# Kernel optimization log

Measured on AMD Instinct MI355X. Metric: run time of the kernel, lower is better.

Reference implementation:

```python
import jax, jax.numpy as jnp
import numpy as np

B = 128          # batch_size
D = 512          # in_features / hidden_size
V = 10000        # word_length (vocab)
T = 20           # sequence_length


def setup_inputs() -> dict:
    key = jax.random.key(0)
    ks = jax.random.split(key, 11)
    s = 0.02
    return {
        "input_": jax.random.normal(ks[0], (1, B, D), dtype=jnp.float32),
        # layer 0 LSTM: input_size=V, hidden_size=D (torch gate order i,f,g,o)
        "W_ih0": jax.random.normal(ks[1], (4 * D, V), dtype=jnp.float32) * s,
        "W_hh0": jax.random.normal(ks[2], (4 * D, D), dtype=jnp.float32) * s,
        "b_ih0": jax.random.normal(ks[3], (4 * D,), dtype=jnp.float32) * s,
        "b_hh0": jax.random.normal(ks[4], (4 * D,), dtype=jnp.float32) * s,
        # layer 1 LSTM: input_size=D, hidden_size=D
        "W_ih1": jax.random.normal(ks[5], (4 * D, D), dtype=jnp.float32) * s,
        "W_hh1": jax.random.normal(ks[6], (4 * D, D), dtype=jnp.float32) * s,
        "b_ih1": jax.random.normal(ks[7], (4 * D,), dtype=jnp.float32) * s,
        "b_hh1": jax.random.normal(ks[8], (4 * D,), dtype=jnp.float32) * s,
        # state_encoder: Linear(D -> V)
        "W_enc": jax.random.normal(ks[9], (V, D), dtype=jnp.float32) * s,
        "b_enc": jax.random.normal(ks[10], (V,), dtype=jnp.float32) * s,
    }


def _lstm_cell(x, h, c, W_ih, W_hh, b_ih, b_hh):
    # x: (B, In), h/c: (B, H). Torch nn.LSTM gate order: i, f, g, o.
    gates = x @ W_ih.T + h @ W_hh.T + (b_ih + b_hh)
    i, f, g, o = jnp.split(gates, 4, axis=-1)
    c_new = jax.nn.sigmoid(f) * c + jax.nn.sigmoid(i) * jnp.tanh(g)
    h_new = jax.nn.sigmoid(o) * jnp.tanh(c_new)
    return h_new, c_new


def reference(input_, W_ih0, W_hh0, b_ih0, b_hh0,
              W_ih1, W_hh1, b_ih1, b_hh1, W_enc, b_enc):
    # Initial states: H[0] = image features, everything else zero;
    # the first timestep input to layer 0 is zeros(B, V).
    h0 = input_[0]                           # (B, D)
    c0 = jnp.zeros_like(h0)
    h1 = jnp.zeros_like(h0)
    c1 = jnp.zeros_like(h0)
    prev_out = jnp.zeros((h0.shape[0], W_ih0.shape[1]), dtype=h0.dtype)  # (B, V)

    def step(carry, _):
        h0, c0, h1, c1, prev = carry
        h0, c0 = _lstm_cell(prev, h0, c0, W_ih0, W_hh0, b_ih0, b_hh0)
        h1, c1 = _lstm_cell(h0, h1, c1, W_ih1, W_hh1, b_ih1, b_hh1)
        out = h1 @ W_enc.T + b_enc           # state_encoder(H[-1]) -> (B, V)
        return (h0, c0, h1, c1, out), out

    _, outs = jax.lax.scan(step, (h0, c0, h1, c1, prev_out), None, length=T)
    return outs                              # (T, B, V) == torch.cat(dim=0)
```

## Files before the change

### kernel.cpp

```cpp
#include <hip/hip_runtime.h>

typedef __attribute__((ext_vector_type(8))) short short8;
typedef __attribute__((ext_vector_type(4))) short short4v;
typedef __attribute__((ext_vector_type(4))) float floatx4;

#define B_   128
#define D_   512
#define V_   10000
#define T_   20
#define G4   2048
#define VPAD 10112
#define KP2  10240
#define BD   (B_*D_)

__device__ __forceinline__ unsigned short f2b(float x){
  union { float f; unsigned u; } c; c.f = x;
  unsigned u = c.u;
  unsigned r = (u + 0x7fffu + ((u>>16)&1u)) >> 16;
  return (unsigned short)r;
}
__device__ __forceinline__ float sigm(float x){ return 1.0f/(1.0f+__expf(-x)); }

__global__ void k_convert(const float* __restrict__ src, unsigned short* __restrict__ dst, int n){
  int i = blockIdx.x*256 + threadIdx.x;
  if (i < n) dst[i] = f2b(src[i]);
}

__global__ void k_prep(const float* __restrict__ Whh0, const float* __restrict__ Wih1,
                       const float* __restrict__ Whh1, const float* __restrict__ input_,
                       const float* __restrict__ b_ih1, const float* __restrict__ b_hh1,
                       unsigned short* __restrict__ Whh0_b, unsigned short* __restrict__ Wih1_b,
                       unsigned short* __restrict__ Whh1_b, unsigned short* __restrict__ h0b0,
                       float* __restrict__ bias1, float* __restrict__ Mf32,
                       unsigned* __restrict__ bar){
  int i = blockIdx.x*256 + threadIdx.x;
  const int NW = G4*512;
  if (i < NW){
    Whh0_b[i] = f2b(Whh0[i]);
    Wih1_b[i] = f2b(Wih1[i]);
    Whh1_b[i] = f2b(Whh1[i]);
    Mf32[i] = 0.f;
  }
  if (i < BD) h0b0[i] = f2b(input_[i]);
  if (i < 2048) bias1[i] = b_ih1[i] + b_hh1[i];
  if (i < 40*8*16) bar[i] = 0u;
}

__global__ __launch_bounds__(256) void k_trans(const float* __restrict__ Wenc,
    unsigned short* __restrict__ Wenc_b, unsigned short* __restrict__ WencT){
  __shared__ short T[64*72];
  int tid = threadIdx.x;
  int v0 = blockIdx.x * 64;
  int d0 = blockIdx.y * 64;
  #pragma unroll
  for (int i=0;i<4;i++){
    int s = tid + 256*i;
    int row = s >> 4, fq = s & 15;
    int v = v0 + row, d = d0 + fq*4;
    float4 f = {0.f,0.f,0.f,0.f};
    if (v < V_) f = *(const float4*)(Wenc + (long)v*D_ + d);
    short4v h; h[0]=(short)f2b(f.x); h[1]=(short)f2b(f.y); h[2]=(short)f2b(f.z); h[3]=(short)f2b(f.w);
    *(short4v*)(&T[row*72 + fq*4]) = h;
    if (v < VPAD) *(short4v*)(Wenc_b + (long)v*D_ + d) = h;
  }
  __syncthreads();
  #pragma unroll
  for (int i=0;i<2;i++){
    int s = tid + 256*i;
    int drow = s >> 3, oct = s & 7;
    short8 v8;
    #pragma unroll
    for (int j=0;j<8;j++) v8[j] = T[(oct*8+j)*72 + drow];
    *(short8*)(WencT + (long)(d0+drow)*KP2 + v0 + oct*8) = v8;
  }
}

__global__ void k_bias_fold(const float* __restrict__ Wih0, const float* __restrict__ b_enc,
                            const float* __restrict__ b_ih0, const float* __restrict__ b_hh0,
                            float* __restrict__ biasA0, float* __restrict__ bfold){
  __shared__ float red[256];
  int g = blockIdx.x;
  const float* row = Wih0 + (long)g*V_;
  float s = 0.f;
  for (int v = threadIdx.x; v < V_; v += 256) s += row[v]*b_enc[v];
  red[threadIdx.x] = s; __syncthreads();
  for (int w = 128; w >= 1; w >>= 1){
    if (threadIdx.x < w) red[threadIdx.x] += red[threadIdx.x+w];
    __syncthreads();
  }
  if (threadIdx.x == 0){
    float ba = b_ih0[g] + b_hh0[g];
    biasA0[g] = ba;
    bfold[g]  = ba + red[0];
  }
}

__global__ __launch_bounds__(256) void k_fold_gemm(const float* __restrict__ A,
                 const unsigned short* __restrict__ BT, float* __restrict__ Mf32){
  __shared__ short At[128*40];
  __shared__ short Bt[128*40];
  int tid = threadIdx.x;
  int b = blockIdx.x;
  int ks = b >> 6, mn = b & 63;
  int bm = mn >> 2, bn = mn & 3;
  int m0 = bm*128, n0 = bn*128, kb = ks*2560;
  int lane = tid&63, wave = tid>>6, l15 = lane&15, quad = lane>>4;
  int wm = (wave>>1)*64, wn = (wave&1)*64;
  floatx4 acc[4][4];
  #pragma unroll
  for (int i=0;i<4;i++)
    #pragma unroll
    for(int j=0;j<4;j++){ floatx4 z = {0.f,0.f,0.f,0.f}; acc[i][j] = z; }
  for (int it = 0; it < 80; it++){
    int k0 = kb + it*32;
    #pragma unroll
    for (int i=0;i<2;i++){
      int slot = tid + 256*i;
      int row = slot >> 2, oct = slot & 3;
      const float* src = A + (long)(m0+row)*V_ + k0 + oct*8;
      short8 v;
      if (k0 + 32 <= V_){
        float4 f0 = *(const float4*)src;
        float4 f1 = *(const float4*)(src+4);
        v[0]=(short)f2b(f0.x); v[1]=(short)f2b(f0.y); v[2]=(short)f2b(f0.z); v[3]=(short)f2b(f0.w);
        v[4]=(short)f2b(f1.x); v[5]=(short)f2b(f1.y); v[6]=(short)f2b(f1.z); v[7]=(short)f2b(f1.w);
      } else {
        #pragma unroll
        for (int j=0;j<8;j++){
          int kk = k0 + oct*8 + j;
          float x = (kk < V_) ? src[j] : 0.f;
          v[j] = (short)f2b(x);
        }
      }
      *(short8*)(&At[row*40 + oct*8]) = v;
    }
    #pragma unroll
    for (int i=0;i<2;i++){
      int slot = tid + 256*i;
      int row = slot >> 2, oct = slot & 3;
      *(short8*)(&Bt[row*40 + oct*8]) = *(const short8*)(BT + (long)(n0+row)*KP2 + k0 + oct*8);
    }
    __syncthreads();
    short8 af[4], bf[4];
    #pragma unroll
    for (int i=0;i<4;i++){
      af[i] = *(const short8*)(&At[(wm + i*16 + l15)*40 + quad*8]);
      bf[i] = *(const short8*)(&Bt[(wn + i*16 + l15)*40 + quad*8]);
    }
    #pragma unroll
    for (int mi=0;mi<4;mi++)
      #pragma unroll
      for (int ni=0;ni<4;ni++)
        acc[mi][ni] = __builtin_amdgcn_mfma_f32_16x16x32_bf16(af[mi],bf[ni],acc[mi][ni],0,0,0);
    __syncthreads();
  }
  #pragma unroll
  for (int mi=0;mi<4;mi++)
    #pragma unroll
    for (int ni=0;ni<4;ni++){
      int n = n0 + wn + ni*16 + l15;
      #pragma unroll
      for (int r=0;r<4;r++){
        int m = m0 + wm + mi*16 + quad*4 + r;
        atomicAdd(&Mf32[(long)m*D_ + n], acc[mi][ni][r]);
      }
    }
}


#define LSTRIDE 520
#define LDS_TILE (32*LSTRIDE)

__device__ __forceinline__ void wait_phase(const unsigned* __restrict__ bar, int p, int tid){
  if (tid < 64){
    const unsigned* cp = bar + (p*8 + (tid&7))*16;
    bool ok;
    do {
      unsigned v = 16u;
      if (tid < 8) v = __hip_atomic_load(cp, __ATOMIC_RELAXED, __HIP_MEMORY_SCOPE_AGENT);
      ok = __all(v >= 16u) != 0;
      if (!ok) __builtin_amdgcn_s_sleep(1);
    } while (!ok);
  }
  __syncthreads();
  asm volatile("" ::: "memory");
}

__device__ __forceinline__ void arrive_phase(unsigned* __restrict__ bar, int p, int slot, int tid){
  asm volatile("s_waitcnt vmcnt(0) lgkmcnt(0)" ::: "memory");
  __syncthreads();
  if (tid == 0)
    __hip_atomic_fetch_add(bar + (p*8 + slot)*16, 1u, __ATOMIC_RELAXED, __HIP_MEMORY_SCOPE_AGENT);
}

__device__ __forceinline__ void stage_tile(const unsigned short* __restrict__ src,
                                           short* __restrict__ dst, int br0, int tid){
  unsigned long long u[16];
  #pragma unroll
  for (int i=0;i<8;i++){
    int c = tid + 256*i;
    int r = c >> 6, o = c & 63;
    const unsigned long long* p = (const unsigned long long*)(src + (long)(br0 + r)*512 + o*8);
    u[2*i]   = __hip_atomic_load(p,   __ATOMIC_RELAXED, __HIP_MEMORY_SCOPE_SYSTEM);
    u[2*i+1] = __hip_atomic_load(p+1, __ATOMIC_RELAXED, __HIP_MEMORY_SCOPE_SYSTEM);
  }
  #pragma unroll
  for (int i=0;i<8;i++){
    int c = tid + 256*i;
    int r = c >> 6, o = c & 63;
    unsigned long long* q = (unsigned long long*)(dst + r*LSTRIDE + o*8);
    q[0] = u[2*i]; q[1] = u[2*i+1];
  }
}

__global__ __launch_bounds__(256, 1) void k_lstm_all(
    const unsigned short* __restrict__ Mfold, const unsigned short* __restrict__ Whh0,
    const unsigned short* __restrict__ Wih1, const unsigned short* __restrict__ Whh1,
    const float* __restrict__ biasA0, const float* __restrict__ bfold,
    const float* __restrict__ bias1,
    unsigned short* __restrict__ h0b0, unsigned short* __restrict__ h0b1,
    unsigned short* __restrict__ Hs, unsigned* __restrict__ bar)
{
  __shared__ short smem[2*LDS_TILE];
  short* ldsA = smem;
  short* ldsB = smem + LDS_TILE;

  int tid = threadIdx.x;
  int L   = blockIdx.x >> 7;
  int idx = blockIdx.x & 127;
  int jg = idx & 31, bs = idx >> 5;
  int br0 = bs*32, j0 = jg*16;
  int slot = idx & 7;
  int lane = tid & 63, wave = tid >> 6;
  int l15 = lane & 15, quad = lane >> 4;

  const unsigned short* WA = (L==0) ? Mfold : Wih1;
  const unsigned short* WB = (L==0) ? Whh0  : Whh1;
  int gRow = wave*512 + j0 + l15;
  short8 bfa[16], bfb[16];
  #pragma unroll
  for (int ks=0; ks<16; ks++){
    bfa[ks] = *(const short8*)(WA + (long)gRow*512 + ks*32 + quad*8);
    bfb[ks] = *(const short8*)(WB + (long)gRow*512 + ks*32 + quad*8);
  }

  int bl = tid >> 3, jjp = (tid & 7)*2;
  int jglob = j0 + jjp;
  float b0g[4][2], bNg[4][2];
  #pragma unroll
  for (int gg=0; gg<4; gg++)
    #pragma unroll
    for (int q=0; q<2; q++){
      if (L==0){
        b0g[gg][q] = biasA0[gg*512 + jglob + q];
        bNg[gg][q] = bfold [gg*512 + jglob + q];
      } else {
        b0g[gg][q] = bias1 [gg*512 + jglob + q];
        bNg[gg][q] = b0g[gg][q];
      }
    }

  float creg[2] = {0.f, 0.f};
  unsigned short* bufs[2] = {h0b0, h0b1};

  for (int t = 0; t < T_; t++){
    const unsigned short *haP, *hbP; unsigned short* hoP;
    bool hasA, hasB; int p_own, p_oth, p_arr;
    if (L == 0){
      haP = (t>0) ? (Hs + (size_t)(t-1)*BD) : nullptr;
      hbP = bufs[t&1];
      hoP = bufs[(t+1)&1];
      hasA = (t>0); hasB = true;
      p_own = 2*(t-1); p_oth = 2*(t-1)+1; p_arr = 2*t;
    } else {
      haP = bufs[(t+1)&1];
      hbP = (t>0) ? (Hs + (size_t)(t-1)*BD) : nullptr;
      hoP = Hs + (size_t)t*BD;
      hasA = true; hasB = (t>0);
      p_own = 2*(t-1)+1; p_oth = 2*t; p_arr = 2*t+1;
    }

    if (hasB){
      if (t > 0) wait_phase(bar, p_own, tid);
      stage_tile(hbP, ldsB, br0, tid);
    }
    if (hasA){
      wait_phase(bar, p_oth, tid);
      stage_tile(haP, ldsA, br0, tid);
    }
    __syncthreads();

    floatx4 acc[2];
    #pragma unroll
    for (int i=0;i<2;i++){ floatx4 z = {0.f,0.f,0.f,0.f}; acc[i] = z; }
    if (hasA){
      #pragma unroll
      for (int ks=0; ks<16; ks++)
        #pragma unroll
        for (int mt=0; mt<2; mt++){
          short8 a = *(const short8*)(ldsA + (mt*16 + l15)*LSTRIDE + ks*32 + quad*8);
          acc[mt] = __builtin_amdgcn_mfma_f32_16x16x32_bf16(a, bfa[ks], acc[mt], 0,0,0);
        }
    }
    if (hasB){
      #pragma unroll
      for (int ks=0; ks<16; ks++)
        #pragma unroll
        for (int mt=0; mt<2; mt++){
          short8 a = *(const short8*)(ldsB + (mt*16 + l15)*LSTRIDE + ks*32 + quad*8);
          acc[mt] = __builtin_amdgcn_mfma_f32_16x16x32_bf16(a, bfb[ks], acc[mt], 0,0,0);
        }
    }
    __syncthreads();

    float* ex = (float*)smem;
    #pragma unroll
    for (int mt=0; mt<2; mt++)
      #pragma unroll
      for (int r=0; r<4; r++)
        ex[wave*512 + (mt*16 + quad*4 + r)*16 + l15] = acc[mt][r];
    __syncthreads();

    {
      float h2[2];
      #pragma unroll
      for (int q=0; q<2; q++){
        float bi = (t==0) ? b0g[0][q] : bNg[0][q];
        float bf_ = (t==0) ? b0g[1][q] : bNg[1][q];
        float bg = (t==0) ? b0g[2][q] : bNg[2][q];
        float bo = (t==0) ? b0g[3][q] : bNg[3][q];
        float gi = ex[0*512 + bl*16 + jjp+q] + bi;
        float gf = ex[1*512 + bl*16 + jjp+q] + bf_;
        float gg = ex[2*512 + bl*16 + jjp+q] + bg;
        float go = ex[3*512 + bl*16 + jjp+q] + bo;
        float ig = sigm(gi), fg = sigm(gf), gt = tanhf(gg), og = sigm(go);
        float cn = fg*creg[q] + ig*gt;
        creg[q] = cn;
        h2[q] = og*tanhf(cn);
      }
      unsigned pack = (unsigned)f2b(h2[0]) | ((unsigned)f2b(h2[1]) << 16);
      __hip_atomic_store((unsigned*)(hoP + (long)(br0 + bl)*512 + jglob), pack,
                         __ATOMIC_RELAXED, __HIP_MEMORY_SCOPE_SYSTEM);
    }
    arrive_phase(bar, p_arr, slot, tid);
  }
}

__global__ __launch_bounds__(256) void k_out_gemm(
    const unsigned short* __restrict__ Ah,
    const unsigned short* __restrict__ Bw,
    const float* __restrict__ b_enc, float* __restrict__ out)
{
  __shared__ short At[128*40];
  __shared__ short Bt[128*40];
  int tid = threadIdx.x;
  int bm = blockIdx.x % 20, bn = blockIdx.x / 20;
  int m0 = bm*128, n0 = bn*128;
  int lane = tid&63, wave = tid>>6, l15 = lane&15, quad = lane>>4;
  int wm = (wave>>1)*64, wn = (wave&1)*64;
  floatx4 acc[4][4];
  #pragma unroll
  for (int i=0;i<4;i++)
    #pragma unroll
    for(int j=0;j<4;j++){ floatx4 z = {0.f,0.f,0.f,0.f}; acc[i][j] = z; }
  for (int k0=0;k0<512;k0+=32){
    #pragma unroll
    for (int i=0;i<2;i++){
      int cc = tid + 256*i; int row = cc>>2; int ko=(cc&3)*8;
      *(short8*)(&At[row*40+ko]) = *(const short8*)(Ah + (long)(m0+row)*512 + k0+ko);
      *(short8*)(&Bt[row*40+ko]) = *(const short8*)(Bw + (long)(n0+row)*512 + k0+ko);
    }
    __syncthreads();
    short8 af[4], bf[4];
    #pragma unroll
    for (int i=0;i<4;i++){
      af[i] = *(const short8*)(&At[(wm + i*16 + l15)*40 + quad*8]);
      bf[i] = *(const short8*)(&Bt[(wn + i*16 + l15)*40 + quad*8]);
    }
    #pragma unroll
    for (int mi=0;mi<4;mi++)
      #pragma unroll
      for (int ni=0;ni<4;ni++)
        acc[mi][ni] = __builtin_amdgcn_mfma_f32_16x16x32_bf16(af[mi],bf[ni],acc[mi][ni],0,0,0);
    __syncthreads();
  }
  #pragma unroll
  for (int mi=0;mi<4;mi++)
    #pragma unroll
    for (int ni=0;ni<4;ni++){
      int n = n0 + wn + ni*16 + l15;
      if (n < V_){
        float be = b_enc[n];
        #pragma unroll
        for (int r=0;r<4;r++){
          int m = m0 + wm + mi*16 + quad*4 + r;
          out[(long)m*V_ + n] = acc[mi][ni][r] + be;
        }
      }
    }
}

extern "C" void kernel_launch(void* const* d_in, const int* in_sizes, int n_in,
                              void* d_out, int out_size, void* d_ws, size_t ws_size,
                              hipStream_t stream){
  const float* input_ = (const float*)d_in[0];
  const float* W_ih0  = (const float*)d_in[1];
  const float* W_hh0  = (const float*)d_in[2];
  const float* b_ih0  = (const float*)d_in[3];
  const float* b_hh0  = (const float*)d_in[4];
  const float* W_ih1  = (const float*)d_in[5];
  const float* W_hh1  = (const float*)d_in[6];
  const float* b_ih1  = (const float*)d_in[7];
  const float* b_hh1  = (const float*)d_in[8];
  const float* W_enc  = (const float*)d_in[9];
  const float* b_enc  = (const float*)d_in[10];
  float* out = (float*)d_out;

  char* ws = (char*)d_ws;
  size_t off = 0;
  auto alloc = [&](size_t bytes){ void* p = ws + off; off += (bytes + 255) & ~255ull; return p; };
  unsigned short* Wenc_b  = (unsigned short*)alloc((size_t)VPAD*512*2);
  unsigned short* WencT_b = (unsigned short*)alloc((size_t)512*KP2*2);
  float*          Mf32    = (float*)alloc((size_t)G4*512*4);
  unsigned short* Mfold_b = (unsigned short*)alloc((size_t)G4*512*2);
  unsigned short* Whh0_b  = (unsigned short*)alloc((size_t)G4*512*2);
  unsigned short* Wih1_b  = (unsigned short*)alloc((size_t)G4*512*2);
  unsigned short* Whh1_b  = (unsigned short*)alloc((size_t)G4*512*2);
  unsigned short* Hs_b    = (unsigned short*)alloc((size_t)T_*BD*2);
  unsigned short* h0b0    = (unsigned short*)alloc((size_t)BD*2);
  unsigned short* h0b1    = (unsigned short*)alloc((size_t)BD*2);
  float* biasA0 = (float*)alloc(2048*4);
  float* bfold  = (float*)alloc(2048*4);
  float* bias1  = (float*)alloc(2048*4);
  unsigned* bar = (unsigned*)alloc((size_t)40*8*16*4);

  k_prep<<<4096, 256, 0, stream>>>(W_hh0, W_ih1, W_hh1, input_, b_ih1, b_hh1,
                                   Whh0_b, Wih1_b, Whh1_b, h0b0, bias1, Mf32, bar);
  k_trans<<<dim3(KP2/64, 512/64), 256, 0, stream>>>(W_enc, Wenc_b, WencT_b);
  k_bias_fold<<<2048, 256, 0, stream>>>(W_ih0, b_enc, b_ih0, b_hh0, biasA0, bfold);
  k_fold_gemm<<<256, 256, 0, stream>>>(W_ih0, WencT_b, Mf32);
  k_convert<<<(G4*512+255)/256, 256, 0, stream>>>(Mf32, Mfold_b, G4*512);

  {
    const unsigned short* a0 = Mfold_b; const unsigned short* a1 = Whh0_b;
    const unsigned short* a2 = Wih1_b; const unsigned short* a3 = Whh1_b;
    const float* a4 = biasA0; const float* a5 = bfold; const float* a6 = bias1;
    unsigned short* a7 = h0b0; unsigned short* a8 = h0b1; unsigned short* a9 = Hs_b;
    unsigned* a10 = bar;
    void* args[] = {&a0,&a1,&a2,&a3,&a4,&a5,&a6,&a7,&a8,&a9,&a10};
    hipLaunchCooperativeKernel((void*)k_lstm_all, dim3(256), dim3(256), args, 0u, stream);
  }

  k_out_gemm<<<20*79, 256, 0, stream>>>(Hs_b, Wenc_b, b_enc, out);
}
```

Before: 666.2 us.

## Replace counter barriers with per-batch-slice flag waits and overlap recurrent MFMA

The LSTM phase barrier is rewritten so each block sets its own flag per phase and batch slice, and waiters check only the 32 flags of their 32-row batch slice instead of global counters summed over all blocks. The recurrent (own-layer) matmul now starts as soon as its input is ready, before waiting on the other layer's input, so more compute overlaps the wait. The fold GEMM block index mapping is also reordered for better L2 locality. This narrows dependencies and may cut stall time, but uses system-scope flag loads and more flag memory.

```diff
diff --git a/kernel.cpp b/kernel.cpp
--- a/kernel.cpp
+++ b/kernel.cpp
@@ -43,7 +43,7 @@
   }
   if (i < BD) h0b0[i] = f2b(input_[i]);
   if (i < 2048) bias1[i] = b_ih1[i] + b_hh1[i];
-  if (i < 40*8*16) bar[i] = 0u;
+  if (i < 40*4*32) bar[i] = 0u;
 }
 
 __global__ __launch_bounds__(256) void k_trans(const float* __restrict__ Wenc,
@@ -101,8 +101,10 @@
   __shared__ short Bt[128*40];
   int tid = threadIdx.x;
   int b = blockIdx.x;
-  int ks = b >> 6, mn = b & 63;
-  int bm = mn >> 2, bn = mn & 3;
+  int x = b & 7;
+  int bn = (b >> 3) & 3;
+  int idx = (b >> 5) * 8 + x;
+  int bm = idx & 15, ks = idx >> 4;
   int m0 = bm*128, n0 = bn*128, kb = ks*2560;
   int lane = tid&63, wave = tid>>6, l15 = lane&15, quad = lane>>4;
   int wm = (wave>>1)*64, wn = (wave&1)*64;
@@ -128,8 +130,8 @@
         #pragma unroll
         for (int j=0;j<8;j++){
           int kk = k0 + oct*8 + j;
-          float x = (kk < V_) ? src[j] : 0.f;
-          v[j] = (short)f2b(x);
+          float xx = (kk < V_) ? src[j] : 0.f;
+          v[j] = (short)f2b(xx);
         }
       }
       *(short8*)(&At[row*40 + oct*8]) = v;
@@ -171,14 +173,13 @@
 #define LSTRIDE 520
 #define LDS_TILE (32*LSTRIDE)
 
-__device__ __forceinline__ void wait_phase(const unsigned* __restrict__ bar, int p, int tid){
+__device__ __forceinline__ void wait_flags(const unsigned* __restrict__ fl, int tid){
   if (tid < 64){
-    const unsigned* cp = bar + (p*8 + (tid&7))*16;
     bool ok;
     do {
-      unsigned v = 16u;
-      if (tid < 8) v = __hip_atomic_load(cp, __ATOMIC_RELAXED, __HIP_MEMORY_SCOPE_AGENT);
-      ok = __all(v >= 16u) != 0;
+      unsigned v = 1u;
+      if (tid < 32) v = __hip_atomic_load(fl + tid, __ATOMIC_RELAXED, __HIP_MEMORY_SCOPE_SYSTEM);
+      ok = (__all(v != 0u) != 0);
       if (!ok) __builtin_amdgcn_s_sleep(1);
     } while (!ok);
   }
@@ -186,11 +187,11 @@
   asm volatile("" ::: "memory");
 }
 
-__device__ __forceinline__ void arrive_phase(unsigned* __restrict__ bar, int p, int slot, int tid){
+__device__ __forceinline__ void set_flag(unsigned* __restrict__ fp, int tid){
   asm volatile("s_waitcnt vmcnt(0) lgkmcnt(0)" ::: "memory");
   __syncthreads();
   if (tid == 0)
-    __hip_atomic_fetch_add(bar + (p*8 + slot)*16, 1u, __ATOMIC_RELAXED, __HIP_MEMORY_SCOPE_AGENT);
+    __hip_atomic_store(fp, 1u, __ATOMIC_RELAXED, __HIP_MEMORY_SCOPE_SYSTEM);
 }
 
 __device__ __forceinline__ void stage_tile(const unsigned short* __restrict__ src,
@@ -230,7 +231,6 @@
   int idx = blockIdx.x & 127;
   int jg = idx & 31, bs = idx >> 5;
   int br0 = bs*32, j0 = jg*16;
-  int slot = idx & 7;
   int lane = tid & 63, wave = tid >> 6;
   int l15 = lane & 15, quad = lane >> 4;
 
@@ -280,35 +280,32 @@
       p_own = 2*(t-1)+1; p_oth = 2*t; p_arr = 2*t+1;
     }
 
+    floatx4 acc[2];
+    #pragma unroll
+    for (int i=0;i<2;i++){ floatx4 z = {0.f,0.f,0.f,0.f}; acc[i] = z; }
+
     if (hasB){
-      if (t > 0) wait_phase(bar, p_own, tid);
+      if (t > 0) wait_flags(bar + (p_own*4 + bs)*32, tid);
       stage_tile(hbP, ldsB, br0, tid);
+      __syncthreads();
+      #pragma unroll
+      for (int ks=0; ks<16; ks++)
+        #pragma unroll
+        for (int mt=0; mt<2; mt++){
+          short8 a = *(const short8*)(ldsB + (mt*16 + l15)*LSTRIDE + ks*32 + quad*8);
+          acc[mt] = __builtin_amdgcn_mfma_f32_16x16x32_bf16(a, bfb[ks], acc[mt], 0,0,0);
+        }
     }
     if (hasA){
-      wait_phase(bar, p_oth, tid);
+      wait_flags(bar + (p_oth*4 + bs)*32, tid);
       stage_tile(haP, ldsA, br0, tid);
-    }
-    __syncthreads();
-
-    floatx4 acc[2];
-    #pragma unroll
-    for (int i=0;i<2;i++){ floatx4 z = {0.f,0.f,0.f,0.f}; acc[i] = z; }
-    if (hasA){
+      __syncthreads();
       #pragma unroll
       for (int ks=0; ks<16; ks++)
         #pragma unroll
         for (int mt=0; mt<2; mt++){
           short8 a = *(const short8*)(ldsA + (mt*16 + l15)*LSTRIDE + ks*32 + quad*8);
           acc[mt] = __builtin_amdgcn_mfma_f32_16x16x32_bf16(a, bfa[ks], acc[mt], 0,0,0);
-        }
-    }
-    if (hasB){
-      #pragma unroll
-      for (int ks=0; ks<16; ks++)
-        #pragma unroll
-        for (int mt=0; mt<2; mt++){
-          short8 a = *(const short8*)(ldsB + (mt*16 + l15)*LSTRIDE + ks*32 + quad*8);
-          acc[mt] = __builtin_amdgcn_mfma_f32_16x16x32_bf16(a, bfb[ks], acc[mt], 0,0,0);
         }
     }
     __syncthreads();
@@ -342,7 +339,7 @@
       __hip_atomic_store((unsigned*)(hoP + (long)(br0 + bl)*512 + jglob), pack,
                          __ATOMIC_RELAXED, __HIP_MEMORY_SCOPE_SYSTEM);
     }
-    arrive_phase(bar, p_arr, slot, tid);
+    set_flag(bar + (p_arr*4 + bs)*32 + jg, tid);
   }
 }
 
@@ -432,7 +429,7 @@
   float* biasA0 = (float*)alloc(2048*4);
   float* bfold  = (float*)alloc(2048*4);
   float* bias1  = (float*)alloc(2048*4);
-  unsigned* bar = (unsigned*)alloc((size_t)40*8*16*4);
+  unsigned* bar = (unsigned*)alloc((size_t)40*4*32*4);
 
   k_prep<<<4096, 256, 0, stream>>>(W_hh0, W_ih1, W_hh1, input_, b_ih1, b_hh1,
                                    Whh0_b, Wih1_b, Whh1_b, h0b0, bias1, Mf32, bar);
```

After: 631.9 us. -5.1%, faster.
